# Optimization experiments

Hardware: AMD Instinct MI355X
Metric: run time of the kernel (lower is better)

## Reference

```python
import jax, jax.numpy as jnp
import numpy as np
from jax import lax

B, T, D, H = 64, 512, 512, 512

def setup_inputs() -> dict:
    key = jax.random.key(0)
    k1, k2, k3, k4 = jax.random.split(key, 4)
    inputs = jax.random.normal(k1, (B, T, D), dtype=jnp.float32)
    kernel = jax.random.normal(k2, (D, 4 * H), dtype=jnp.float32) * 0.05
    recurrent_kernel = jax.random.normal(k3, (H, 4 * H), dtype=jnp.float32) * 0.05
    bias = jnp.zeros((4 * H,), dtype=jnp.float32)
    init_h = jnp.zeros((B, H), dtype=jnp.float32)
    init_c = jnp.zeros((B, H), dtype=jnp.float32)
    mask = jax.random.randint(k4, (B, T), 0, 2) > 0  # bool [B,T]
    return {"inputs": inputs, "init_h": init_h, "init_c": init_c,
            "kernel": kernel, "recurrent_kernel": recurrent_kernel,
            "bias": bias, "mask": mask}


def _lstm(inputs, init_h, init_c, kernel, recurrent_kernel, bias, mask):
    # batch-major -> time-major, as the _rnn driver does (swap_batch_timestep)
    x = jnp.transpose(inputs, (1, 0, 2))            # [T,B,D]
    m = jnp.transpose(mask, (1, 0))[:, :, None]     # [T,B,1]
    # Input projection is linear in x: precompute once (same math as per-step)
    xz = jnp.einsum('tbd,dg->tbg', x, kernel) + bias  # [T,B,4H]

    def step(carry, xs):
        h, c, prev_out = carry
        z_x, m_t = xs
        z = z_x + h @ recurrent_kernel              # [B,4H]
        zi, zf, zg, zo = jnp.split(z, 4, axis=-1)   # Keras gate order i,f,g,o
        i = jax.nn.sigmoid(zi)
        f = jax.nn.sigmoid(zf)
        g = jnp.tanh(zg)
        o = jax.nn.sigmoid(zo)
        c_new = f * c + i * g
        h_new = o * jnp.tanh(c_new)
        # masking semantics of _rnn: carry previous output/state where masked
        out = jnp.where(m_t, h_new, prev_out)
        h2 = jnp.where(m_t, h_new, h)
        c2 = jnp.where(m_t, c_new, c)
        return (h2, c2, out), out

    init = (init_h, init_c, jnp.zeros_like(init_h))
    (h_f, c_f, _), outs = lax.scan(step, init, (xz, m))
    outputs = jnp.transpose(outs, (1, 0, 2))        # back to [B,T,H]
    return outputs, h_f, c_f


def reference(inputs, init_h, init_c, kernel, recurrent_kernel, bias, mask):
    return _lstm(inputs, init_h, init_c, kernel, recurrent_kernel, bias, mask)
```

## Files before the change

kernel.cpp:

```cpp
#include <hip/hip_runtime.h>

constexpr int BB = 64, TT = 512, DD = 512, HH = 512;
constexpr int GG = 4 * HH;
constexpr int KK = DD + HH;
constexpr int NBLK = 128, NTHR = 512;
constexpr int LDS_ZL = 4 * 16 * 129 * 4;
constexpr int LDS_BYTES = 8192 + 8192 + LDS_ZL + 512;

using short8 = __attribute__((ext_vector_type(8))) short;
using f32x4  = __attribute__((ext_vector_type(4))) float;

__device__ __host__ __forceinline__ unsigned short f2bf(float f) {
    union { float f; unsigned u; } v; v.f = f;
    unsigned u = v.u + 0x7fffu + ((v.u >> 16) & 1u);
    return (unsigned short)(u >> 16);
}
__device__ __forceinline__ float fsig(float x) {
    return 1.f / (1.f + __expf(-x));
}
__device__ __forceinline__ float ftanh_(float x) {
    float e = __expf(2.f * fabsf(x));
    float r = 1.f - 2.f / (e + 1.f);
    return copysignf(r, x);
}


__global__ void prep_kernel(const float* __restrict__ Wx,
                            const float* __restrict__ Wr,
                            const float* __restrict__ init_h,
                            const int*   __restrict__ mask,
                            unsigned short* __restrict__ WB,
                            unsigned* __restrict__ hbuf0,
                            unsigned* __restrict__ flags,
                            unsigned* __restrict__ mpack) {
    int idx = blockIdx.x * blockDim.x + threadIdx.x;
    if (idx < GG * KK) {
        int g = idx >> 10, k = idx & 1023;
        float v = (k < DD) ? Wx[(size_t)k * GG + g]
                           : Wr[(size_t)(k - DD) * GG + g];
        WB[idx] = f2bf(v);
    }
    if (idx < BB * HH / 2) {
        int b = idx >> 8, p = idx & 255;
        unsigned lo = f2bf(init_h[b * HH + 2 * p]);
        unsigned hi = f2bf(init_h[b * HH + 2 * p + 1]);
        hbuf0[(b >> 3) * 4096 + (b & 7) * 256 + p] = lo | (hi << 16);
    }
    if (idx < 2048) flags[idx] = 0u;
    if (idx < 64 * 16) {
        int b = idx >> 4, w = idx & 15;
        unsigned word = 0u;
        for (int tb = 0; tb < 32; ++tb)
            word |= (mask[b * TT + w * 32 + tb] != 0 ? 1u : 0u) << tb;
        mpack[idx] = word;
    }
}

__global__ void __launch_bounds__(NTHR, 1)
lstm_kernel(const float* __restrict__ x,
            const unsigned short* __restrict__ WB,
            const float* __restrict__ bias,
            unsigned*    hbuf,
            unsigned*    flags,
            const unsigned* __restrict__ mpack,
            const float* __restrict__ init_h,
            const float* __restrict__ init_c,
            float* __restrict__ out)
{
    extern __shared__ char smem[];
    char*     smx   = smem;
    char*     smh   = smem + 8192;
    float*    zlp   = (float*)(smem + 16384);
    unsigned* m_lds = (unsigned*)(smem + 16384 + LDS_ZL);

    const int tid = threadIdx.x;
    const int bid = blockIdx.x;
    const int w   = tid >> 6;
    const int l   = tid & 63;
    const int kq  = w >> 1;
    const int nh  = w & 1;

    const int grp    = bid & 7;
    const int qb     = bid >> 3;
    const int j_base = qb * 32;
    const int obase  = grp * 8;

    short8 bf[8][4];
    #pragma unroll
    for (int nt = 0; nt < 4; ++nt) {
        int n   = nh * 4 + nt;
        int col = n * 16 + (l & 15);
        int g   = (col >> 5) * 512 + j_base + (col & 31);
        const unsigned short* wrow = WB + (size_t)g * KK + (l >> 4) * 8;
        #pragma unroll
        for (int i = 0; i < 4; ++i) {
            bf[i][nt]     = *(const short8*)(wrow + (kq * 4 + i) * 32);
            bf[4 + i][nt] = *(const short8*)(wrow + (16 + kq * 4 + i) * 32);
        }
    }

    const int m_u = tid >> 5, jl = tid & 31;
    const int b_glob = obase + m_u;
    const int jg = j_base + jl;
    float c_reg = 0.f, h_reg = 0.f, po_reg = 0.f;
    float bias_r[4] = {0.f, 0.f, 0.f, 0.f};
    if (tid < 256) {
        c_reg = init_c[b_glob * HH + jg];
        h_reg = init_h[b_glob * HH + jg];
        #pragma unroll
        for (int gt = 0; gt < 4; ++gt) bias_r[gt] = bias[gt * 512 + jg];
    }
    for (int i = tid; i < 128; i += NTHR)
        m_lds[i] = mpack[(obase + (i >> 4)) * 16 + (i & 15)];

    unsigned* hgrp = hbuf + grp * 4096;
    const size_t OUT_HF = (size_t)BB * TT * HH;
    const size_t OUT_CF = OUT_HF + (size_t)BB * HH;
    const int arow = l & 7;
    const int rsw  = arow << 4;

    for (int u = tid; u < 512; u += NTHR) {
        int row = u >> 6, c = u & 63;
        const float4* xp = (const float4*)(
            x + ((size_t)(obase + row) * TT + 0) * DD + 8 * c);
        float4 f0 = xp[0], f1 = xp[1];
        short8 v;
        v[0] = (short)f2bf(f0.x); v[1] = (short)f2bf(f0.y);
        v[2] = (short)f2bf(f0.z); v[3] = (short)f2bf(f0.w);
        v[4] = (short)f2bf(f1.x); v[5] = (short)f2bf(f1.y);
        v[6] = (short)f2bf(f1.z); v[7] = (short)f2bf(f1.w);
        *(short8*)(smx + row * 1024 + ((16 * c) ^ ((row & 7) << 4))) = v;
    }
    __syncthreads();

    for (int t = 0; t < TT; ++t) {
        {
            const unsigned tgt = (unsigned)t;
            const unsigned* fb = flags + grp * 256 + (l & 15) * 16;
            for (;;) {
                unsigned v = __hip_atomic_load(fb, __ATOMIC_RELAXED,
                                               __HIP_MEMORY_SCOPE_AGENT);
                if (__all(v >= tgt)) break;
                __builtin_amdgcn_s_sleep(1);
            }
        }

        const unsigned* curb = hgrp + (size_t)(t & 1) * 2048;
        unsigned*       nxtb = hgrp + (size_t)((t + 1) & 1) * 2048;
        uint4 hv;
        {
            const unsigned* hp = curb + w * 256 + l * 4;
            asm volatile("global_load_dwordx4 %0, %1, off sc1"
                         : "=v"(hv) : "v"(hp) : "memory");
        }

        f32x4 acc[4] = {{0,0,0,0},{0,0,0,0},{0,0,0,0},{0,0,0,0}};
        #pragma unroll
        for (int i = 0; i < 4; ++i) {
            int kt = kq * 4 + i;
            short8 a = *(const short8*)(
                smx + arow * 1024 + ((kt * 64 + (l >> 4) * 16) ^ rsw));
            #pragma unroll
            for (int nt = 0; nt < 4; ++nt)
                acc[nt] = __builtin_amdgcn_mfma_f32_16x16x32_bf16(a, bf[i][nt], acc[nt], 0, 0, 0);
        }

        asm volatile("s_waitcnt vmcnt(0)" ::: "memory");
        __builtin_amdgcn_sched_barrier(0);
        {
            union { uint4 u; short8 s; } cv; cv.u = hv;
            *(short8*)(smh + w * 1024 + ((l * 16) ^ ((w & 7) << 4))) = cv.s;
        }
        __syncthreads();

        #pragma unroll
        for (int i = 0; i < 4; ++i) {
            int kt = kq * 4 + i;
            short8 a = *(const short8*)(
                smh + arow * 1024 + ((kt * 64 + (l >> 4) * 16) ^ rsw));
            #pragma unroll
            for (int nt = 0; nt < 4; ++nt)
                acc[nt] = __builtin_amdgcn_mfma_f32_16x16x32_bf16(a, bf[4 + i][nt], acc[nt], 0, 0, 0);
        }
        if ((l >> 4) < 2) {
            #pragma unroll
            for (int nt = 0; nt < 4; ++nt) {
                int n = nh * 4 + nt;
                #pragma unroll
                for (int r = 0; r < 4; ++r) {
                    int m = (l >> 4) * 4 + r;
                    zlp[(kq * 16 + m) * 129 + n * 16 + (l & 15)] = acc[nt][r];
                }
            }
        }
        __syncthreads();

        if (tid < 256) {
            bool msk = ((m_lds[m_u * 16 + (t >> 5)] >> (t & 31)) & 1u) != 0u;
            float z[4];
            #pragma unroll
            for (int gt = 0; gt < 4; ++gt) {
                float s = bias_r[gt];
                #pragma unroll
                for (int p = 0; p < 4; ++p)
                    s += zlp[(p * 16 + m_u) * 129 + gt * 32 + jl];
                z[gt] = s;
            }
            float ig = fsig(z[0]);
            float fg = fsig(z[1]);
            float gg = ftanh_(z[2]);
            float og = fsig(z[3]);
            float c_new = fg * c_reg + ig * gg;
            float h_new = og * ftanh_(c_new);
            float ov = msk ? h_new : po_reg;
            float h2 = msk ? h_new : h_reg;
            float c2 = msk ? c_new : c_reg;
            out[((size_t)b_glob * TT + t) * HH + jg] = ov;
            unsigned hb16 = f2bf(h2);
            unsigned other = (unsigned)__shfl_xor((int)hb16, 1);
            if ((jl & 1) == 0)
                __hip_atomic_store(nxtb + m_u * 256 + qb * 16 + (jl >> 1),
                                   hb16 | (other << 16), __ATOMIC_RELAXED,
                                   __HIP_MEMORY_SCOPE_AGENT);
            c_reg = c2; h_reg = h2; po_reg = ov;
        } else if (t + 1 < TT) {
            for (int u = tid - 256; u < 512; u += 256) {
                int row = u >> 6, c = u & 63;
                const float4* xp = (const float4*)(
                    x + ((size_t)(obase + row) * TT + (t + 1)) * DD + 8 * c);
                float4 f0 = xp[0], f1 = xp[1];
                short8 v;
                v[0] = (short)f2bf(f0.x); v[1] = (short)f2bf(f0.y);
                v[2] = (short)f2bf(f0.z); v[3] = (short)f2bf(f0.w);
                v[4] = (short)f2bf(f1.x); v[5] = (short)f2bf(f1.y);
                v[6] = (short)f2bf(f1.z); v[7] = (short)f2bf(f1.w);
                *(short8*)(smx + row * 1024 + ((16 * c) ^ ((row & 7) << 4))) = v;
            }
        }
        __syncthreads();

        if (tid == 0)
            __hip_atomic_store(flags + (grp * 16 + qb) * 16, (unsigned)(t + 1),
                               __ATOMIC_RELAXED, __HIP_MEMORY_SCOPE_AGENT);
    }

    if (tid < 256) {
        out[OUT_HF + (size_t)b_glob * HH + jg] = h_reg;
        out[OUT_CF + (size_t)b_glob * HH + jg] = c_reg;
    }
}

extern "C" void kernel_launch(void* const* d_in, const int* in_sizes, int n_in,
                              void* d_out, int out_size, void* d_ws, size_t ws_size,
                              hipStream_t stream) {
    const float* x      = (const float*)d_in[0];
    const float* init_h = (const float*)d_in[1];
    const float* init_c = (const float*)d_in[2];
    const float* Wx     = (const float*)d_in[3];
    const float* Wr     = (const float*)d_in[4];
    const float* bias   = (const float*)d_in[5];
    const int*   mask   = (const int*)d_in[6];
    float* out = (float*)d_out;

    unsigned short* WB    = (unsigned short*)d_ws;
    unsigned*       hbuf  = (unsigned*)(WB + (size_t)GG * KK);
    unsigned*       flags = hbuf + 8 * 4096;
    unsigned*       mpack = flags + 2048;

    prep_kernel<<<(GG * KK + 255) / 256, 256, 0, stream>>>(
        Wx, Wr, init_h, mask, WB, hbuf, flags, mpack);

    void* args[] = { (void*)&x, (void*)&WB, (void*)&bias, (void*)&hbuf,
                     (void*)&flags, (void*)&mpack, (void*)&init_h,
                     (void*)&init_c, (void*)&out };
    (void)hipLaunchCooperativeKernel((const void*)lstm_kernel, dim3(NBLK),
                                     dim3(NTHR), args, (unsigned)LDS_BYTES,
                                     stream);
}
```

Baseline: 1.385 ms.

## Give each wave full-K ownership of gate columns to drop LDS split-K reduction

Each wave now owns 16 interleaved gate columns (4 hidden units × 4 gates) across the full K dimension, holding 32 bf16 weight fragments in registers. This removes the cross-wave split-K partial sums in LDS, together with one __syncthreads per timestep. Gate values are exchanged with lane shuffles, and the cell update runs in the MFMA lanes. In exchange, each wave runs a longer serial chain of 32 MFMAs on a single accumulator, and only half of each wave's lanes do the pointwise work. The next-step x load is also spread across all threads.

```diff
diff --git a/kernel.cpp b/kernel.cpp
--- a/kernel.cpp
+++ b/kernel.cpp
@@ -4,8 +4,7 @@
 constexpr int GG = 4 * HH;
 constexpr int KK = DD + HH;
 constexpr int NBLK = 128, NTHR = 512;
-constexpr int LDS_ZL = 4 * 16 * 129 * 4;
-constexpr int LDS_BYTES = 8192 + 8192 + LDS_ZL + 512;
+constexpr int LDS_BYTES = 8192 + 8192 + 512;
 
 using short8 = __attribute__((ext_vector_type(8))) short;
 using f32x4  = __attribute__((ext_vector_type(4))) float;
@@ -70,45 +69,43 @@
     extern __shared__ char smem[];
     char*     smx   = smem;
     char*     smh   = smem + 8192;
-    float*    zlp   = (float*)(smem + 16384);
-    unsigned* m_lds = (unsigned*)(smem + 16384 + LDS_ZL);
+    unsigned* m_lds = (unsigned*)(smem + 16384);
 
     const int tid = threadIdx.x;
     const int bid = blockIdx.x;
     const int w   = tid >> 6;
     const int l   = tid & 63;
-    const int kq  = w >> 1;
-    const int nh  = w & 1;
 
     const int grp    = bid & 7;
     const int qb     = bid >> 3;
     const int j_base = qb * 32;
     const int obase  = grp * 8;
 
-    short8 bf[8][4];
-    #pragma unroll
-    for (int nt = 0; nt < 4; ++nt) {
-        int n   = nh * 4 + nt;
-        int col = n * 16 + (l & 15);
-        int g   = (col >> 5) * 512 + j_base + (col & 31);
+    short8 bf[32];
+    {
+        int n = l & 15;
+        int g = (n & 3) * 512 + j_base + w * 4 + (n >> 2);
         const unsigned short* wrow = WB + (size_t)g * KK + (l >> 4) * 8;
         #pragma unroll
-        for (int i = 0; i < 4; ++i) {
-            bf[i][nt]     = *(const short8*)(wrow + (kq * 4 + i) * 32);
-            bf[4 + i][nt] = *(const short8*)(wrow + (16 + kq * 4 + i) * 32);
-        }
-    }
-
-    const int m_u = tid >> 5, jl = tid & 31;
-    const int b_glob = obase + m_u;
-    const int jg = j_base + jl;
-    float c_reg = 0.f, h_reg = 0.f, po_reg = 0.f;
-    float bias_r[4] = {0.f, 0.f, 0.f, 0.f};
-    if (tid < 256) {
-        c_reg = init_c[b_glob * HH + jg];
-        h_reg = init_h[b_glob * HH + jg];
-        #pragma unroll
-        for (int gt = 0; gt < 4; ++gt) bias_r[gt] = bias[gt * 512 + jg];
+        for (int kt = 0; kt < 32; ++kt)
+            bf[kt] = *(const short8*)(wrow + kt * 32);
+    }
+
+    const int gt   = l & 3;
+    const int jlw  = (l >> 2) & 3;
+    const int jloc = w * 4 + jlw;
+    const int jg   = j_base + jloc;
+    const int rq   = (l >> 4) & 1;
+    float c_reg[4] = {0,0,0,0}, h_reg[4] = {0,0,0,0}, po_reg[4] = {0,0,0,0};
+    float bz = 0.f;
+    if (l < 32) {
+        bz = bias[gt * 512 + jg];
+        #pragma unroll
+        for (int r = 0; r < 4; ++r) {
+            int row_g = obase + rq * 4 + r;
+            c_reg[r] = init_c[row_g * HH + jg];
+            h_reg[r] = init_h[row_g * HH + jg];
+        }
     }
     for (int i = tid; i < 128; i += NTHR)
         m_lds[i] = mpack[(obase + (i >> 4)) * 16 + (i & 15)];
@@ -119,8 +116,8 @@
     const int arow = l & 7;
     const int rsw  = arow << 4;
 
-    for (int u = tid; u < 512; u += NTHR) {
-        int row = u >> 6, c = u & 63;
+    {
+        int row = tid >> 6, c = tid & 63;
         const float4* xp = (const float4*)(
             x + ((size_t)(obase + row) * TT + 0) * DD + 8 * c);
         float4 f0 = xp[0], f1 = xp[1];
@@ -154,15 +151,12 @@
                          : "=v"(hv) : "v"(hp) : "memory");
         }
 
-        f32x4 acc[4] = {{0,0,0,0},{0,0,0,0},{0,0,0,0},{0,0,0,0}};
-        #pragma unroll
-        for (int i = 0; i < 4; ++i) {
-            int kt = kq * 4 + i;
+        f32x4 acc = {0.f, 0.f, 0.f, 0.f};
+        #pragma unroll
+        for (int kt = 0; kt < 16; ++kt) {
             short8 a = *(const short8*)(
                 smx + arow * 1024 + ((kt * 64 + (l >> 4) * 16) ^ rsw));
-            #pragma unroll
-            for (int nt = 0; nt < 4; ++nt)
-                acc[nt] = __builtin_amdgcn_mfma_f32_16x16x32_bf16(a, bf[i][nt], acc[nt], 0, 0, 0);
+            acc = __builtin_amdgcn_mfma_f32_16x16x32_bf16(a, bf[kt], acc, 0, 0, 0);
         }
 
         asm volatile("s_waitcnt vmcnt(0)" ::: "memory");
@@ -174,68 +168,63 @@
         __syncthreads();
 
         #pragma unroll
-        for (int i = 0; i < 4; ++i) {
-            int kt = kq * 4 + i;
+        for (int kt = 0; kt < 16; ++kt) {
             short8 a = *(const short8*)(
                 smh + arow * 1024 + ((kt * 64 + (l >> 4) * 16) ^ rsw));
+            acc = __builtin_amdgcn_mfma_f32_16x16x32_bf16(a, bf[16 + kt], acc, 0, 0, 0);
+        }
+
+        if (l < 32) {
+            bool msk[4];
             #pragma unroll
-            for (int nt = 0; nt < 4; ++nt)
-                acc[nt] = __builtin_amdgcn_mfma_f32_16x16x32_bf16(a, bf[4 + i][nt], acc[nt], 0, 0, 0);
-        }
-        if ((l >> 4) < 2) {
+            for (int r = 0; r < 4; ++r)
+                msk[r] = ((m_lds[(rq * 4 + r) * 16 + (t >> 5)] >> (t & 31)) & 1u) != 0u;
+            float hnew[4], ov[4];
             #pragma unroll
-            for (int nt = 0; nt < 4; ++nt) {
-                int n = nh * 4 + nt;
-                #pragma unroll
-                for (int r = 0; r < 4; ++r) {
-                    int m = (l >> 4) * 4 + r;
-                    zlp[(kq * 16 + m) * 129 + n * 16 + (l & 15)] = acc[nt][r];
+            for (int r = 0; r < 4; ++r) {
+                float z  = acc[r] + bz;
+                float v1 = __shfl_xor(z, 1);
+                float v2 = __shfl_xor(z, 2);
+                float v3 = __shfl_xor(v1, 2);
+                float zi = gt == 0 ? z  : gt == 1 ? v1 : gt == 2 ? v2 : v3;
+                float zf = gt == 0 ? v1 : gt == 1 ? z  : gt == 2 ? v3 : v2;
+                float zg = gt == 0 ? v2 : gt == 1 ? v3 : gt == 2 ? z  : v1;
+                float zo = gt == 0 ? v3 : gt == 1 ? v2 : gt == 2 ? v1 : z;
+                float ig = fsig(zi), fg = fsig(zf);
+                float gg = ftanh_(zg), og = fsig(zo);
+                float c_new = fg * c_reg[r] + ig * gg;
+                float h_new = og * ftanh_(c_new);
+                ov[r]   = msk[r] ? h_new : po_reg[r];
+                hnew[r] = msk[r] ? h_new : h_reg[r];
+                c_reg[r]  = msk[r] ? c_new : c_reg[r];
+                h_reg[r]  = hnew[r];
+                po_reg[r] = ov[r];
+            }
+            out[((size_t)(obase + rq * 4 + gt) * TT + t) * HH + jg] = ov[gt];
+            #pragma unroll
+            for (int r = 0; r < 4; ++r) {
+                float hp1 = __shfl_xor(hnew[r], 4);
+                if ((l & 7) == 0) {
+                    unsigned pv = (unsigned)f2bf(hnew[r])
+                                | ((unsigned)f2bf(hp1) << 16);
+                    __hip_atomic_store(nxtb + (rq * 4 + r) * 256 + qb * 16 + (jloc >> 1),
+                                       pv, __ATOMIC_RELAXED,
+                                       __HIP_MEMORY_SCOPE_AGENT);
                 }
             }
         }
-        __syncthreads();
-
-        if (tid < 256) {
-            bool msk = ((m_lds[m_u * 16 + (t >> 5)] >> (t & 31)) & 1u) != 0u;
-            float z[4];
-            #pragma unroll
-            for (int gt = 0; gt < 4; ++gt) {
-                float s = bias_r[gt];
-                #pragma unroll
-                for (int p = 0; p < 4; ++p)
-                    s += zlp[(p * 16 + m_u) * 129 + gt * 32 + jl];
-                z[gt] = s;
-            }
-            float ig = fsig(z[0]);
-            float fg = fsig(z[1]);
-            float gg = ftanh_(z[2]);
-            float og = fsig(z[3]);
-            float c_new = fg * c_reg + ig * gg;
-            float h_new = og * ftanh_(c_new);
-            float ov = msk ? h_new : po_reg;
-            float h2 = msk ? h_new : h_reg;
-            float c2 = msk ? c_new : c_reg;
-            out[((size_t)b_glob * TT + t) * HH + jg] = ov;
-            unsigned hb16 = f2bf(h2);
-            unsigned other = (unsigned)__shfl_xor((int)hb16, 1);
-            if ((jl & 1) == 0)
-                __hip_atomic_store(nxtb + m_u * 256 + qb * 16 + (jl >> 1),
-                                   hb16 | (other << 16), __ATOMIC_RELAXED,
-                                   __HIP_MEMORY_SCOPE_AGENT);
-            c_reg = c2; h_reg = h2; po_reg = ov;
-        } else if (t + 1 < TT) {
-            for (int u = tid - 256; u < 512; u += 256) {
-                int row = u >> 6, c = u & 63;
-                const float4* xp = (const float4*)(
-                    x + ((size_t)(obase + row) * TT + (t + 1)) * DD + 8 * c);
-                float4 f0 = xp[0], f1 = xp[1];
-                short8 v;
-                v[0] = (short)f2bf(f0.x); v[1] = (short)f2bf(f0.y);
-                v[2] = (short)f2bf(f0.z); v[3] = (short)f2bf(f0.w);
-                v[4] = (short)f2bf(f1.x); v[5] = (short)f2bf(f1.y);
-                v[6] = (short)f2bf(f1.z); v[7] = (short)f2bf(f1.w);
-                *(short8*)(smx + row * 1024 + ((16 * c) ^ ((row & 7) << 4))) = v;
-            }
+
+        if (t + 1 < TT) {
+            int row = tid >> 6, c = tid & 63;
+            const float4* xp = (const float4*)(
+                x + ((size_t)(obase + row) * TT + (t + 1)) * DD + 8 * c);
+            float4 f0 = xp[0], f1 = xp[1];
+            short8 v;
+            v[0] = (short)f2bf(f0.x); v[1] = (short)f2bf(f0.y);
+            v[2] = (short)f2bf(f0.z); v[3] = (short)f2bf(f0.w);
+            v[4] = (short)f2bf(f1.x); v[5] = (short)f2bf(f1.y);
+            v[6] = (short)f2bf(f1.z); v[7] = (short)f2bf(f1.w);
+            *(short8*)(smx + row * 1024 + ((16 * c) ^ ((row & 7) << 4))) = v;
         }
         __syncthreads();
 
@@ -244,9 +233,10 @@
                                __ATOMIC_RELAXED, __HIP_MEMORY_SCOPE_AGENT);
     }
 
-    if (tid < 256) {
-        out[OUT_HF + (size_t)b_glob * HH + jg] = h_reg;
-        out[OUT_CF + (size_t)b_glob * HH + jg] = c_reg;
+    if (l < 32) {
+        int row_g = obase + rq * 4 + gt;
+        out[OUT_HF + (size_t)row_g * HH + jg] = h_reg[gt];
+        out[OUT_CF + (size_t)row_g * HH + jg] = c_reg[gt];
     }
 }
 
```

New measurement: 2.212 ms. 59.7% more time.

## Split K in halves per wave, prefetch x via registers, use per-wave flags

Applied to the files above, without the earlier changes.

Reorganizes the MFMA work so each wave covers half of K and two N tiles, which halves the partial-sum buffer and the reduction in the gate step. The next timestep's x rows are now loaded by all threads into registers, overlapped with the MFMAs, and converted with packed bf16 instructions. The trailing block barrier is removed: each gate wave publishes its own flag after its h stores complete, and consumers poll 64 per-wave flags. This shortens the per-step critical path but depends on raw store ordering through sc1 and vmcnt waits for correctness across blocks.

```diff
diff --git a/kernel.cpp b/kernel.cpp
--- a/kernel.cpp
+++ b/kernel.cpp
@@ -4,7 +4,7 @@
 constexpr int GG = 4 * HH;
 constexpr int KK = DD + HH;
 constexpr int NBLK = 128, NTHR = 512;
-constexpr int LDS_ZL = 4 * 16 * 129 * 4;
+constexpr int LDS_ZL = 16 * 129 * 4;
 constexpr int LDS_BYTES = 8192 + 8192 + LDS_ZL + 512;
 
 using short8 = __attribute__((ext_vector_type(8))) short;
@@ -46,7 +46,7 @@
         unsigned hi = f2bf(init_h[b * HH + 2 * p + 1]);
         hbuf0[(b >> 3) * 4096 + (b & 7) * 256 + p] = lo | (hi << 16);
     }
-    if (idx < 2048) flags[idx] = 0u;
+    if (idx < 512) flags[idx] = 0u;
     if (idx < 64 * 16) {
         int b = idx >> 4, w = idx & 15;
         unsigned word = 0u;
@@ -77,25 +77,25 @@
     const int bid = blockIdx.x;
     const int w   = tid >> 6;
     const int l   = tid & 63;
-    const int kq  = w >> 1;
-    const int nh  = w & 1;
+    const int kh  = w >> 2;
+    const int ng  = w & 3;
 
     const int grp    = bid & 7;
     const int qb     = bid >> 3;
     const int j_base = qb * 32;
     const int obase  = grp * 8;
 
-    short8 bf[8][4];
+    short8 bf[16][2];
     #pragma unroll
-    for (int nt = 0; nt < 4; ++nt) {
-        int n   = nh * 4 + nt;
+    for (int nt = 0; nt < 2; ++nt) {
+        int n   = ng * 2 + nt;
         int col = n * 16 + (l & 15);
         int g   = (col >> 5) * 512 + j_base + (col & 31);
         const unsigned short* wrow = WB + (size_t)g * KK + (l >> 4) * 8;
         #pragma unroll
-        for (int i = 0; i < 4; ++i) {
-            bf[i][nt]     = *(const short8*)(wrow + (kq * 4 + i) * 32);
-            bf[4 + i][nt] = *(const short8*)(wrow + (16 + kq * 4 + i) * 32);
+        for (int i = 0; i < 8; ++i) {
+            bf[i][nt]     = *(const short8*)(wrow + (kh * 8 + i) * 32);
+            bf[8 + i][nt] = *(const short8*)(wrow + (16 + kh * 8 + i) * 32);
         }
     }
 
@@ -118,27 +118,29 @@
     const size_t OUT_CF = OUT_HF + (size_t)BB * HH;
     const int arow = l & 7;
     const int rsw  = arow << 4;
-
-    for (int u = tid; u < 512; u += NTHR) {
-        int row = u >> 6, c = u & 63;
+    const int xrow_s = tid >> 6;
+    const int xcol_s = tid & 63;
+
+    {
         const float4* xp = (const float4*)(
-            x + ((size_t)(obase + row) * TT + 0) * DD + 8 * c);
+            x + ((size_t)(obase + xrow_s) * TT + 0) * DD + 8 * xcol_s);
         float4 f0 = xp[0], f1 = xp[1];
         short8 v;
         v[0] = (short)f2bf(f0.x); v[1] = (short)f2bf(f0.y);
         v[2] = (short)f2bf(f0.z); v[3] = (short)f2bf(f0.w);
         v[4] = (short)f2bf(f1.x); v[5] = (short)f2bf(f1.y);
         v[6] = (short)f2bf(f1.z); v[7] = (short)f2bf(f1.w);
-        *(short8*)(smx + row * 1024 + ((16 * c) ^ ((row & 7) << 4))) = v;
+        *(short8*)(smx + xrow_s * 1024 +
+                   ((16 * xcol_s) ^ ((xrow_s & 7) << 4))) = v;
     }
     __syncthreads();
 
     for (int t = 0; t < TT; ++t) {
         {
             const unsigned tgt = (unsigned)t;
-            const unsigned* fb = flags + grp * 256 + (l & 15) * 16;
+            const unsigned* fb = flags + grp * 64;
             for (;;) {
-                unsigned v = __hip_atomic_load(fb, __ATOMIC_RELAXED,
+                unsigned v = __hip_atomic_load(fb + l, __ATOMIC_RELAXED,
                                                __HIP_MEMORY_SCOPE_AGENT);
                 if (__all(v >= tgt)) break;
                 __builtin_amdgcn_s_sleep(1);
@@ -147,25 +149,33 @@
 
         const unsigned* curb = hgrp + (size_t)(t & 1) * 2048;
         unsigned*       nxtb = hgrp + (size_t)((t + 1) & 1) * 2048;
-        uint4 hv;
+        uint4 hv, xv0, xv1;
         {
             const unsigned* hp = curb + w * 256 + l * 4;
             asm volatile("global_load_dwordx4 %0, %1, off sc1"
                          : "=v"(hv) : "v"(hp) : "memory");
         }
-
-        f32x4 acc[4] = {{0,0,0,0},{0,0,0,0},{0,0,0,0},{0,0,0,0}};
-        #pragma unroll
-        for (int i = 0; i < 4; ++i) {
-            int kt = kq * 4 + i;
+        if (t + 1 < TT) {
+            const float* xrp = x + ((size_t)(obase + xrow_s) * TT + (t + 1)) * DD
+                                 + 8 * xcol_s;
+            asm volatile("global_load_dwordx4 %0, %2, off\n\t"
+                         "global_load_dwordx4 %1, %3, off"
+                         : "=&v"(xv0), "=&v"(xv1)
+                         : "v"(xrp), "v"(xrp + 4) : "memory");
+        }
+
+        f32x4 acc0 = {0.f, 0.f, 0.f, 0.f}, acc1 = {0.f, 0.f, 0.f, 0.f};
+        #pragma unroll
+        for (int i = 0; i < 8; ++i) {
+            int kt = kh * 8 + i;
             short8 a = *(const short8*)(
                 smx + arow * 1024 + ((kt * 64 + (l >> 4) * 16) ^ rsw));
-            #pragma unroll
-            for (int nt = 0; nt < 4; ++nt)
-                acc[nt] = __builtin_amdgcn_mfma_f32_16x16x32_bf16(a, bf[i][nt], acc[nt], 0, 0, 0);
-        }
-
-        asm volatile("s_waitcnt vmcnt(0)" ::: "memory");
+            acc0 = __builtin_amdgcn_mfma_f32_16x16x32_bf16(a, bf[i][0], acc0, 0, 0, 0);
+            acc1 = __builtin_amdgcn_mfma_f32_16x16x32_bf16(a, bf[i][1], acc1, 0, 0, 0);
+        }
+
+        if (t + 1 < TT) asm volatile("s_waitcnt vmcnt(2)" ::: "memory");
+        else            asm volatile("s_waitcnt vmcnt(0)" ::: "memory");
         __builtin_amdgcn_sched_barrier(0);
         {
             union { uint4 u; short8 s; } cv; cv.u = hv;
@@ -174,38 +184,47 @@
         __syncthreads();
 
         #pragma unroll
-        for (int i = 0; i < 4; ++i) {
-            int kt = kq * 4 + i;
+        for (int i = 0; i < 8; ++i) {
+            int kt = kh * 8 + i;
             short8 a = *(const short8*)(
                 smh + arow * 1024 + ((kt * 64 + (l >> 4) * 16) ^ rsw));
-            #pragma unroll
-            for (int nt = 0; nt < 4; ++nt)
-                acc[nt] = __builtin_amdgcn_mfma_f32_16x16x32_bf16(a, bf[4 + i][nt], acc[nt], 0, 0, 0);
+            acc0 = __builtin_amdgcn_mfma_f32_16x16x32_bf16(a, bf[8 + i][0], acc0, 0, 0, 0);
+            acc1 = __builtin_amdgcn_mfma_f32_16x16x32_bf16(a, bf[8 + i][1], acc1, 0, 0, 0);
         }
         if ((l >> 4) < 2) {
             #pragma unroll
-            for (int nt = 0; nt < 4; ++nt) {
-                int n = nh * 4 + nt;
-                #pragma unroll
-                for (int r = 0; r < 4; ++r) {
-                    int m = (l >> 4) * 4 + r;
-                    zlp[(kq * 16 + m) * 129 + n * 16 + (l & 15)] = acc[nt][r];
-                }
-            }
+            for (int r = 0; r < 4; ++r) {
+                int row = (l >> 4) * 4 + r;
+                zlp[(kh * 8 + row) * 129 + (ng * 2) * 16 + (l & 15)]     = acc0[r];
+                zlp[(kh * 8 + row) * 129 + (ng * 2 + 1) * 16 + (l & 15)] = acc1[r];
+            }
+        }
+
+        if (t + 1 < TT) {
+            asm volatile("s_waitcnt vmcnt(0)" ::: "memory");
+            __builtin_amdgcn_sched_barrier(0);
+            union { uint4 u; float4 f; } xa, xb; xa.u = xv0; xb.u = xv1;
+            unsigned u0, u1, u2, u3;
+            asm("v_cvt_pk_bf16_f32 %0, %1, %2" : "=v"(u0) : "v"(xa.f.x), "v"(xa.f.y));
+            asm("v_cvt_pk_bf16_f32 %0, %1, %2" : "=v"(u1) : "v"(xa.f.z), "v"(xa.f.w));
+            asm("v_cvt_pk_bf16_f32 %0, %1, %2" : "=v"(u2) : "v"(xb.f.x), "v"(xb.f.y));
+            asm("v_cvt_pk_bf16_f32 %0, %1, %2" : "=v"(u3) : "v"(xb.f.z), "v"(xb.f.w));
+            union { unsigned u[4]; short8 s; } cv;
+            cv.u[0] = u0; cv.u[1] = u1; cv.u[2] = u2; cv.u[3] = u3;
+            *(short8*)(smx + xrow_s * 1024 +
+                       ((16 * xcol_s) ^ ((xrow_s & 7) << 4))) = cv.s;
         }
         __syncthreads();
 
         if (tid < 256) {
+            const int wv = tid >> 6;
             bool msk = ((m_lds[m_u * 16 + (t >> 5)] >> (t & 31)) & 1u) != 0u;
             float z[4];
             #pragma unroll
-            for (int gt = 0; gt < 4; ++gt) {
-                float s = bias_r[gt];
-                #pragma unroll
-                for (int p = 0; p < 4; ++p)
-                    s += zlp[(p * 16 + m_u) * 129 + gt * 32 + jl];
-                z[gt] = s;
-            }
+            for (int gt = 0; gt < 4; ++gt)
+                z[gt] = bias_r[gt]
+                      + zlp[m_u * 129 + gt * 32 + jl]
+                      + zlp[(8 + m_u) * 129 + gt * 32 + jl];
             float ig = fsig(z[0]);
             float fg = fsig(z[1]);
             float gg = ftanh_(z[2]);
@@ -216,32 +235,22 @@
             float h2 = msk ? h_new : h_reg;
             float c2 = msk ? c_new : c_reg;
             out[((size_t)b_glob * TT + t) * HH + jg] = ov;
-            unsigned hb16 = f2bf(h2);
-            unsigned other = (unsigned)__shfl_xor((int)hb16, 1);
-            if ((jl & 1) == 0)
-                __hip_atomic_store(nxtb + m_u * 256 + qb * 16 + (jl >> 1),
-                                   hb16 | (other << 16), __ATOMIC_RELAXED,
-                                   __HIP_MEMORY_SCOPE_AGENT);
+            float hp1 = __shfl_xor(h2, 1);
+            if ((jl & 1) == 0) {
+                unsigned pv = (unsigned)f2bf(h2) | ((unsigned)f2bf(hp1) << 16);
+                unsigned* hp = nxtb + m_u * 256 + qb * 16 + (jl >> 1);
+                asm volatile("global_store_dword %0, %1, off sc1"
+                             :: "v"(hp), "v"(pv) : "memory");
+            }
             c_reg = c2; h_reg = h2; po_reg = ov;
-        } else if (t + 1 < TT) {
-            for (int u = tid - 256; u < 512; u += 256) {
-                int row = u >> 6, c = u & 63;
-                const float4* xp = (const float4*)(
-                    x + ((size_t)(obase + row) * TT + (t + 1)) * DD + 8 * c);
-                float4 f0 = xp[0], f1 = xp[1];
-                short8 v;
-                v[0] = (short)f2bf(f0.x); v[1] = (short)f2bf(f0.y);
-                v[2] = (short)f2bf(f0.z); v[3] = (short)f2bf(f0.w);
-                v[4] = (short)f2bf(f1.x); v[5] = (short)f2bf(f1.y);
-                v[6] = (short)f2bf(f1.z); v[7] = (short)f2bf(f1.w);
-                *(short8*)(smx + row * 1024 + ((16 * c) ^ ((row & 7) << 4))) = v;
-            }
-        }
-        __syncthreads();
-
-        if (tid == 0)
-            __hip_atomic_store(flags + (grp * 16 + qb) * 16, (unsigned)(t + 1),
-                               __ATOMIC_RELAXED, __HIP_MEMORY_SCOPE_AGENT);
+            asm volatile("s_waitcnt vmcnt(0)" ::: "memory");
+            if (l == 0) {
+                unsigned* fp = flags + grp * 64 + qb * 4 + wv;
+                unsigned fv = (unsigned)(t + 1);
+                asm volatile("global_store_dword %0, %1, off sc1"
+                             :: "v"(fp), "v"(fv) : "memory");
+            }
+        }
     }
 
     if (tid < 256) {
@@ -265,7 +274,7 @@
     unsigned short* WB    = (unsigned short*)d_ws;
     unsigned*       hbuf  = (unsigned*)(WB + (size_t)GG * KK);
     unsigned*       flags = hbuf + 8 * 4096;
-    unsigned*       mpack = flags + 2048;
+    unsigned*       mpack = flags + 512;
 
     prep_kernel<<<(GG * KK + 255) / 256, 256, 0, stream>>>(
         Wx, Wr, init_h, mask, WB, hbuf, flags, mpack);
```

New measurement: 3.440 ms. 2.48x slower.
